# Kernel tuning notes

Hardware: AMD Instinct MI355X
Metric: run time of the kernel (lower is better)

Reference implementation:

```python
import jax, jax.numpy as jnp
import numpy as np

K = 20
EPS = 1e-5
NEG_SLOPE = 0.2


def _bn(x, gamma, beta, axes):
    # batch-norm in training mode (batch statistics), per-channel on last axis
    mean = jnp.mean(x, axis=axes, keepdims=True)
    var = jnp.var(x, axis=axes, keepdims=True)
    return gamma * (x - mean) * jax.lax.rsqrt(var + EPS) + beta


def _lrelu(x):
    return jnp.where(x >= 0, x, NEG_SLOPE * x)


def setup_inputs() -> dict:
    key = jax.random.key(0)
    ks = jax.random.split(key, 8)
    B, C, N = 8, 6, 4096

    def w(k_, shape):
        fan_in = shape[-1]
        return jax.random.normal(k_, shape, jnp.float32) / np.sqrt(fan_in)

    return {
        "x": jax.random.normal(ks[0], (B, C, N), jnp.float32),
        "conv1_w": w(ks[1], (64, 12)),
        "bn1_g": jnp.ones((64,), jnp.float32), "bn1_b": jnp.zeros((64,), jnp.float32),
        "conv2_w": w(ks[2], (128, 64)),
        "bn2_g": jnp.ones((128,), jnp.float32), "bn2_b": jnp.zeros((128,), jnp.float32),
        "conv3_w": w(ks[3], (1024, 128)),
        "bn3_g": jnp.ones((1024,), jnp.float32), "bn3_b": jnp.zeros((1024,), jnp.float32),
        "fc1_w": w(ks[4], (512, 1024)),
        "bn4_g": jnp.ones((512,), jnp.float32), "bn4_b": jnp.zeros((512,), jnp.float32),
        "fc2_w": w(ks[5], (256, 512)),
        "bn5_g": jnp.ones((256,), jnp.float32), "bn5_b": jnp.zeros((256,), jnp.float32),
        "fc3_w": w(ks[6], (9, 256)), "fc3_b": jnp.zeros((9,), jnp.float32),
        "fc4_w": w(ks[7], (3, 256)), "fc4_b": jnp.zeros((3,), jnp.float32),
    }


def _get_graph_feature(x, k):
    # x: [B, C, N] -> [B, N, k, 2C]
    B, C, N = x.shape
    xt = jnp.transpose(x, (0, 2, 1))                      # [B, N, C]
    xx = jnp.sum(xt * xt, axis=-1)                        # [B, N]
    inner = jnp.einsum('bnc,bmc->bnm', xt, xt)            # [B, N, N]
    pd = 2.0 * inner - xx[:, :, None] - xx[:, None, :]    # -||xi-xj||^2
    _, idx = jax.lax.top_k(pd, k)                         # [B, N, k]
    nbr = xt[jnp.arange(B)[:, None, None], idx]           # [B, N, k, C]
    center = jnp.broadcast_to(xt[:, :, None, :], nbr.shape)
    return jnp.concatenate([nbr - center, center], axis=-1)  # [B, N, k, 2C]


def reference(x, conv1_w, bn1_g, bn1_b, conv2_w, bn2_g, bn2_b,
              conv3_w, bn3_g, bn3_b, fc1_w, bn4_g, bn4_b,
              fc2_w, bn5_g, bn5_b, fc3_w, fc3_b, fc4_w, fc4_b):
    B = x.shape[0]
    feat = _get_graph_feature(x, K)                            # [B, N, k, 12]
    h = _lrelu(_bn(jnp.einsum('bnkc,oc->bnko', feat, conv1_w), bn1_g, bn1_b, (0, 1, 2)))
    h = _lrelu(_bn(jnp.einsum('bnkc,oc->bnko', h, conv2_w), bn2_g, bn2_b, (0, 1, 2)))
    h = jnp.max(h, axis=2)                                     # [B, N, 128] max over k
    h = _lrelu(_bn(jnp.einsum('bnc,oc->bno', h, conv3_w), bn3_g, bn3_b, (0, 1)))
    g = jnp.max(h, axis=1)                                     # [B, 1024] max over points
    g = _lrelu(_bn(g @ fc1_w.T, bn4_g, bn4_b, (0,)))           # [B, 512]
    g = _lrelu(_bn(g @ fc2_w.T, bn5_g, bn5_b, (0,)))           # [B, 256]
    bias = (g @ fc4_w.T + fc4_b)[:, None, :]                   # [B, 1, 3]
    matrix = jnp.eye(3, dtype=x.dtype) + (g @ fc3_w.T + fc3_b).reshape(B, 3, 3)
    xyz = jnp.transpose(x[:, :3, :], (0, 2, 1))                # [B, N, 3]
    out = jnp.einsum('bnc,bcd->bnd', xyz, matrix) + bias       # [B, N, 3]
    return jnp.transpose(out, (0, 2, 1))                       # [B, 3, N]
```

## Files before the change

kernel.cpp:

```cpp
#include <hip/hip_runtime.h>
#include <math.h>
#include <stddef.h>


static constexpr float EPS_ = 1e-5f;

__global__ __launch_bounds__(256) void k_prep(const float* __restrict__ x,
                                              float* __restrict__ xtp,
                                              const float* __restrict__ w2,
                                              float* __restrict__ w2t)
{
    int i = blockIdx.x*256 + threadIdx.x;
    int b = i >> 12, n = i & 4095;
    const float* xb = x + (size_t)b*6*4096 + n;
    float v0 = xb[0], v1 = xb[4096], v2 = xb[2*4096];
    float v3 = xb[3*4096], v4 = xb[4*4096], v5 = xb[5*4096];
    float xx = v0*v0 + v1*v1 + v2*v2 + v3*v3 + v4*v4 + v5*v5;
    float4* o = (float4*)(xtp + (size_t)i*8);
    o[0] = make_float4(v0, v1, v2, v3);
    o[1] = make_float4(v4, v5, xx, 0.f);
    if (blockIdx.x < 2){
        int e = blockIdx.x*256 + threadIdx.x;
        for (int q = e; q < 64*128; q += 512){
            int c = q >> 7, oo = q & 127;
            w2t[q] = w2[oo*64 + c];
        }
    }
}

__device__ __forceinline__ float pd_calc(const float4 a0, const float4 a1,
                                         const float4 q0, const float4 q1)
{
    float dot = a0.x*q0.x;
    dot = fmaf(a0.y, q0.y, dot);
    dot = fmaf(a0.z, q0.z, dot);
    dot = fmaf(a0.w, q0.w, dot);
    dot = fmaf(a1.x, q1.x, dot);
    dot = fmaf(a1.y, q1.y, dot);
    return fmaf(2.f, dot, -a1.z - q1.z);
}

__device__ __forceinline__ unsigned fkey_(float f){
    unsigned u = __float_as_uint(f);
    return (u & 0x80000000u) ? ~u : (u | 0x80000000u);
}
__device__ __forceinline__ float finv_(unsigned k){
    return (k & 0x80000000u) ? __uint_as_float(k & 0x7fffffffu)
                             : __uint_as_float(~k);
}

#define TK_CAP 384
__global__ __launch_bounds__(256) void k_topk(const float* __restrict__ xtp,
                                              int* __restrict__ idxout)
{
    __shared__ float maxs[4][256];
    __shared__ float candv[4][TK_CAP];
    __shared__ int   candi[4][TK_CAP];
    __shared__ float Ts[4];
    __shared__ unsigned ccnt[4], ocnt[4], nwork;
    __shared__ unsigned short work[1024];

    const int t = threadIdx.x;
    const int rowbase = blockIdx.x << 2;
    const int b = rowbase >> 12;
    const float* xb = xtp + ((size_t)b << 15);

    float4 c0[4], c1[4];
    #pragma unroll
    for (int c = 0; c < 4; c++){
        const float4* p = (const float4*)(xtp + (size_t)(rowbase + c)*8);
        c0[c] = p[0]; c1[c] = p[1];
    }
    if (t < 4){ ccnt[t] = 0u; ocnt[t] = 0u; }
    if (t == 0) nwork = 0u;

    float mx[4] = {-INFINITY, -INFINITY, -INFINITY, -INFINITY};
    {
        const float4* qp = (const float4*)(xb + (size_t)t*8);
        for (int i = 0; i < 16; i++){
            float4 q0 = qp[0], q1 = qp[1];
            #pragma unroll
            for (int c = 0; c < 4; c++)
                mx[c] = fmaxf(mx[c], pd_calc(c0[c], c1[c], q0, q1));
            qp += 512;
        }
    }
    #pragma unroll
    for (int c = 0; c < 4; c++) maxs[c][t] = mx[c];
    __syncthreads();

    const int w = t >> 6, lane = t & 63;
    {
        unsigned k0 = fkey_(maxs[w][lane]);
        unsigned k1 = fkey_(maxs[w][64  + lane]);
        unsigned k2 = fkey_(maxs[w][128 + lane]);
        unsigned k3 = fkey_(maxs[w][192 + lane]);
        unsigned lo = 0u;
        for (int bit = 31; bit >= 0; bit--){
            unsigned cand = lo | (1u << bit);
            int cnt = __popcll(__ballot(k0 >= cand))
                    + __popcll(__ballot(k1 >= cand))
                    + __popcll(__ballot(k2 >= cand))
                    + __popcll(__ballot(k3 >= cand));
            if (cnt >= 20) lo = cand;
        }
        if (lane == 0) Ts[w] = finv_(lo);
    }
    __syncthreads();

    #pragma unroll
    for (int c = 0; c < 4; c++){
        if (mx[c] >= Ts[c]){
            unsigned pos = atomicAdd(&nwork, 1u);
            work[pos] = (unsigned short)((c << 8) | t);
        }
    }
    __syncthreads();

    {
        int total = (int)nwork << 4;
        for (int e = t; e < total; e += 256){
            int ct = work[e >> 4];
            int c = ct >> 8, src = ct & 255;
            int m = ((e & 15) << 8) | src;
            const float4* p = (const float4*)(xb + (size_t)m*8);
            float4 q0 = p[0], q1 = p[1];
            float pd = pd_calc(c0[c], c1[c], q0, q1);
            if (pd >= Ts[c]){
                unsigned pos = atomicAdd(&ccnt[c], 1u);
                if (pos < TK_CAP){ candv[c][pos] = pd; candi[c][pos] = m; }
            }
        }
    }
    __syncthreads();

    {
        int n = (int)min(ccnt[w], (unsigned)TK_CAP);
        unsigned key[6]; int id[6];
        #pragma unroll
        for (int j = 0; j < 6; j++){
            int p = (j << 6) | lane;
            bool ok = p < n;
            key[j] = ok ? fkey_(candv[w][p]) : 0u;
            id[j]  = ok ? candi[w][p] : 0x7fffffff;
        }
        unsigned C = 0u;
        for (int bit = 31; bit >= 0; bit--){
            unsigned cand = C | (1u << bit);
            int cnt = 0;
            #pragma unroll
            for (int j = 0; j < 6; j++)
                cnt += __popcll(__ballot(key[j] >= cand));
            if (cnt >= 20) C = cand;
        }
        int m = 0, e = 0;
        #pragma unroll
        for (int j = 0; j < 6; j++){
            m += __popcll(__ballot(key[j] > C));
            e += __popcll(__ballot(key[j] == C));
        }
        int* outp = idxout + (size_t)(rowbase + w)*20;
        #pragma unroll
        for (int j = 0; j < 6; j++){
            if (key[j] > C){
                unsigned pos = atomicAdd(&ocnt[w], 1u);
                outp[pos] = id[j];
            }
        }
        int need = 20 - m;
        if (e <= need){
            #pragma unroll
            for (int j = 0; j < 6; j++){
                if (key[j] == C){
                    unsigned pos = atomicAdd(&ocnt[w], 1u);
                    outp[pos] = id[j];
                }
            }
        } else {
            for (int r = 0; r < need; r++){
                int loc = 0x7fffffff;
                #pragma unroll
                for (int j = 0; j < 6; j++)
                    if (key[j] == C && id[j] < loc) loc = id[j];
                int g = loc;
                #pragma unroll
                for (int s = 1; s < 64; s <<= 1) g = min(g, __shfl_xor(g, s));
                #pragma unroll
                for (int j = 0; j < 6; j++){
                    if (key[j] == C && id[j] == g){
                        key[j] = 0u;
                        unsigned pos = atomicAdd(&ocnt[w], 1u);
                        outp[pos] = g;
                    }
                }
            }
        }
    }
}

__global__ __launch_bounds__(256) void k_bn1stats(const float* __restrict__ xtp,
                                                  const int* __restrict__ idxb,
                                                  const float* __restrict__ w1,
                                                  float* __restrict__ bn1sum,
                                                  float* __restrict__ bn1sq)
{
    __shared__ float fT[320*12];
    __shared__ float red[2][4][64];
    const int t = threadIdx.x;
    const int rowbase = blockIdx.x << 4;
    const int b = rowbase >> 12;

    for (int s = t; s < 320; s += 256){
        int r = s / 20, k = s % 20;
        int grow = rowbase + r;
        int m = idxb[(size_t)grow*20 + k];
        const float4* pn = (const float4*)(xtp + (size_t)((b << 12) | m)*8);
        const float4* pc = (const float4*)(xtp + (size_t)grow*8);
        float4 n0 = pn[0], n1 = pn[1], c0 = pc[0], c1 = pc[1];
        float* f = fT + s*12;
        ((float4*)f)[0] = make_float4(n0.x-c0.x, n0.y-c0.y, n0.z-c0.z, n0.w-c0.w);
        ((float4*)f)[1] = make_float4(n1.x-c1.x, n1.y-c1.y, c0.x, c0.y);
        ((float4*)f)[2] = make_float4(c0.z, c0.w, c1.x, c1.y);
    }
    __syncthreads();
    const int o = t & 63, grp = t >> 6;
    float w[12];
    #pragma unroll
    for (int c = 0; c < 12; c++) w[c] = w1[o*12 + c];
    float sm = 0.f, sq = 0.f;
    for (int s = grp*80; s < grp*80 + 80; s++){
        const float* f = fT + s*12;
        float4 f0 = *(const float4*)(f);
        float4 fa = *(const float4*)(f + 4);
        float4 fb = *(const float4*)(f + 8);
        float h = w[0]*f0.x + w[1]*f0.y + w[2]*f0.z + w[3]*f0.w
                + w[4]*fa.x + w[5]*fa.y + w[6]*fa.z + w[7]*fa.w
                + w[8]*fb.x + w[9]*fb.y + w[10]*fb.z + w[11]*fb.w;
        sm += h; sq = fmaf(h, h, sq);
    }
    red[0][grp][o] = sm; red[1][grp][o] = sq;
    __syncthreads();
    if (t < 64){
        float a = red[0][0][t] + red[0][1][t] + red[0][2][t] + red[0][3][t];
        float c2 = red[1][0][t] + red[1][1][t] + red[1][2][t] + red[1][3][t];
        atomicAdd(bn1sum + t, a);
        atomicAdd(bn1sq + t, c2);
    }
}

__global__ void k_bnfin(const float* __restrict__ sum, const float* __restrict__ sq,
                        const float* __restrict__ gamma, const float* __restrict__ beta,
                        float* __restrict__ st, int C, float invN)
{
    int o = threadIdx.x;
    if (o < C){
        float mean = sum[o]*invN;
        float var  = sq[o]*invN - mean*mean;
        float s = gamma[o]/sqrtf(var + EPS_);
        st[o] = s;
        st[C + o] = beta[o] - mean*s;
    }
}

__global__ __launch_bounds__(256, 3) void k_conv12(
    const float* __restrict__ xtp, const int* __restrict__ idxb,
    const float* __restrict__ w1, const float* __restrict__ w2t,
    const float* __restrict__ bn1st,
    float* __restrict__ h2max, float* __restrict__ bn2sum, float* __restrict__ bn2sq)
{
    __shared__ float f1s[80*64];
    __shared__ float w2u[16*516];
    const int t = threadIdx.x;
    const int rowbase = blockIdx.x << 2;
    const int b = rowbase >> 12;

    const int jch = t & 63;
    float wr[12];
    #pragma unroll
    for (int c = 0; c < 12; c++) wr[c] = w1[jch*12 + c];

    float* fT = w2u;
    if (t < 80){
        int r = t / 20;
        int grow = rowbase + r;
        int m = idxb[(size_t)grow*20 + (t - r*20)];
        const float4* pn = (const float4*)(xtp + (size_t)((b << 12) | m)*8);
        const float4* pc = (const float4*)(xtp + (size_t)grow*8);
        float4 n0 = pn[0], n1 = pn[1], c0 = pc[0], c1 = pc[1];
        float* f = fT + t*12;
        ((float4*)f)[0] = make_float4(n0.x-c0.x, n0.y-c0.y, n0.z-c0.z, n0.w-c0.w);
        ((float4*)f)[1] = make_float4(n1.x-c1.x, n1.y-c1.y, c0.x, c0.y);
        ((float4*)f)[2] = make_float4(c0.z, c0.w, c1.x, c1.y);
    }
    __syncthreads();
    {
        const float s1 = bn1st[jch], t1 = bn1st[64 + jch];
        for (int vid = t; vid < 5120; vid += 256){
            int vec = vid >> 6;
            const float* f = fT + vec*12;
            float4 f0 = *(const float4*)(f);
            float4 fa = *(const float4*)(f + 4);
            float4 fb = *(const float4*)(f + 8);
            float acc = wr[0]*f0.x + wr[1]*f0.y + wr[2]*f0.z + wr[3]*f0.w
                      + wr[4]*fa.x + wr[5]*fa.y + wr[6]*fa.z + wr[7]*fa.w
                      + wr[8]*fb.x + wr[9]*fb.y + wr[10]*fb.z + wr[11]*fb.w;
            float v = fmaf(s1, acc, t1);
            f1s[(vec << 6) + (jch ^ ((vec & 7) << 2))] = fmaxf(v, 0.2f*v);
        }
    }
    __syncthreads();
    {
        float4 tmp[8];
        #pragma unroll
        for (int i = 0; i < 8; i++) tmp[i] = ((const float4*)w2t)[t + (i << 8)];
        #pragma unroll
        for (int i = 0; i < 8; i++){
            int q = t + (i << 8);
            int jr = q >> 5, o4 = q & 31;
            *(float4*)&w2u[(o4 >> 1)*516 + (jr << 3) + ((o4 & 1) << 2)] = tmp[i];
        }
    }
    __syncthreads();

    const int vg = t & 15, og = t >> 4;
    const float* fp = f1s + vg*5*64;
    const float* wp = w2u + og*516;
    int xw[5];
    #pragma unroll
    for (int i = 0; i < 5; i++) xw[i] = ((vg*5 + i) & 7) << 2;

    float h[5][8];
    #pragma unroll
    for (int i = 0; i < 5; i++)
        #pragma unroll
        for (int oi = 0; oi < 8; oi++) h[i][oi] = 0.f;

    #pragma unroll
    for (int jl = 0; jl < 64; jl += 4){
        float wv[4][8];
        #pragma unroll
        for (int jj = 0; jj < 4; jj++){
            *(float4*)&wv[jj][0] = *(const float4*)&wp[((jl + jj) << 3)];
            *(float4*)&wv[jj][4] = *(const float4*)&wp[((jl + jj) << 3) + 4];
        }
        #pragma unroll
        for (int i = 0; i < 5; i++){
            float fv[4];
            *(float4*)fv = *(const float4*)&fp[(i << 6) + (jl ^ xw[i])];
            #pragma unroll
            for (int jj = 0; jj < 4; jj++)
                #pragma unroll
                for (int oi = 0; oi < 8; oi++)
                    h[i][oi] = fmaf(fv[jj], wv[jj][oi], h[i][oi]);
        }
    }

    float mxl[8], sml[8], sql[8];
    #pragma unroll
    for (int oi = 0; oi < 8; oi++){
        float v = h[0][oi];
        mxl[oi] = v; sml[oi] = v; sql[oi] = v*v;
    }
    #pragma unroll
    for (int i = 1; i < 5; i++)
        #pragma unroll
        for (int oi = 0; oi < 8; oi++){
            float v = h[i][oi];
            mxl[oi] = fmaxf(mxl[oi], v);
            sml[oi] += v;
            sql[oi] = fmaf(v, v, sql[oi]);
        }
    __syncthreads();
    {
        const int r = vg >> 2, q = vg & 3;
        int base = (((q << 2) | r) << 7) + (og << 3);
        *(float4*)&w2u[base]        = *(float4*)&mxl[0];
        *(float4*)&w2u[base + 4]    = *(float4*)&mxl[4];
        *(float4*)&w2u[2048 + base]     = *(float4*)&sml[0];
        *(float4*)&w2u[2048 + base + 4] = *(float4*)&sml[4];
        *(float4*)&w2u[4096 + base]     = *(float4*)&sql[0];
        *(float4*)&w2u[4096 + base + 4] = *(float4*)&sql[4];
    }
    __syncthreads();
    for (int it = t; it < 512; it += 256){
        int r = it >> 7, o = it & 127;
        float m = w2u[(r << 7) + o];
        #pragma unroll
        for (int q = 1; q < 4; q++) m = fmaxf(m, w2u[(((q << 2) | r) << 7) + o]);
        h2max[(size_t)(rowbase + r)*128 + o] = m;
    }
    if (t < 128){
        float s = 0.f, qq = 0.f;
        #pragma unroll
        for (int u = 0; u < 16; u++){
            s  += w2u[2048 + (u << 7) + t];
            qq += w2u[4096 + (u << 7) + t];
        }
        atomicAdd(bn2sum + t, s);
        atomicAdd(bn2sq + t, qq);
    }
}

__global__ __launch_bounds__(256) void k_wt3(const float* __restrict__ w3,
                                             float* __restrict__ w3t)
{
    int i = blockIdx.x*256 + threadIdx.x;
    int j = i >> 10, o = i & 1023;
    w3t[i] = w3[(size_t)o*128 + j];
}

__global__ __launch_bounds__(256, 2) void k_conv3(const float* __restrict__ h2max,
    const float* __restrict__ bn2st, const float* __restrict__ w3t,
    float* __restrict__ bn3sum, float* __restrict__ bn3sq, unsigned int* __restrict__ gkey)
{
    __shared__ float f2[64*132];
    __shared__ float w3s[8192];
    const int t = threadIdx.x;
    const int bid = blockIdx.x;
    const int idx = bid >> 3;
    const int rt = (bid & 7)*64 + (idx >> 4);
    const int ot = idx & 15;
    const int rowbase = rt << 6;
    const int obase = ot << 6;
    const int b = rowbase >> 12;

    for (int e = t; e < 64*128; e += 256){
        int r = e >> 7, c = e & 127;
        float v = h2max[(size_t)(rowbase + r)*128 + c];
        float u = fmaf(bn2st[c], v, bn2st[128 + c]);
        f2[r*132 + c] = fmaxf(u, 0.2f*u);
    }
    {
        float4 tmp[8];
        #pragma unroll
        for (int i = 0; i < 8; i++){
            int q = t + (i << 8);
            tmp[i] = *(const float4*)&w3t[(size_t)(q >> 4)*1024 + obase + ((q & 15) << 2)];
        }
        #pragma unroll
        for (int i = 0; i < 8; i++) ((float4*)w3s)[t + (i << 8)] = tmp[i];
    }
    __syncthreads();

    const int oq = t & 15, rg = t >> 4;
    const int o0 = oq << 2, r0 = rg << 2;
    float h[4][4];
    #pragma unroll
    for (int rr = 0; rr < 4; rr++)
        #pragma unroll
        for (int oi = 0; oi < 4; oi++) h[rr][oi] = 0.f;

    for (int jl = 0; jl < 128; jl += 4){
        float wv[4][4];
        #pragma unroll
        for (int jj = 0; jj < 4; jj++)
            *(float4*)wv[jj] = *(const float4*)&w3s[(jl + jj)*64 + o0];
        float fr[4][4];
        #pragma unroll
        for (int rr = 0; rr < 4; rr++)
            *(float4*)fr[rr] = *(const float4*)&f2[(r0 + rr)*132 + jl];
        #pragma unroll
        for (int jj = 0; jj < 4; jj++)
            #pragma unroll
            for (int rr = 0; rr < 4; rr++)
                #pragma unroll
                for (int oi = 0; oi < 4; oi++)
                    h[rr][oi] = fmaf(fr[rr][jj], wv[jj][oi], h[rr][oi]);
    }

    float sml[4], sql[4], mxl[4];
    #pragma unroll
    for (int oi = 0; oi < 4; oi++){
        float v = h[0][oi];
        sml[oi] = v; sql[oi] = v*v; mxl[oi] = v;
    }
    #pragma unroll
    for (int rr = 1; rr < 4; rr++)
        #pragma unroll
        for (int oi = 0; oi < 4; oi++){
            float v = h[rr][oi];
            sml[oi] += v;
            sql[oi] = fmaf(v, v, sql[oi]);
            mxl[oi] = fmaxf(mxl[oi], v);
        }
    __syncthreads();
    float* scr = f2;
    *(float4*)&scr[(rg << 6) + o0]        = *(float4*)&sml[0];
    *(float4*)&scr[1024 + (rg << 6) + o0] = *(float4*)&sql[0];
    *(float4*)&scr[2048 + (rg << 6) + o0] = *(float4*)&mxl[0];
    __syncthreads();
    if (t < 192){
        int stat = t >> 6, o = t & 63;
        if (stat == 0){
            float s = 0.f;
            #pragma unroll
            for (int g2 = 0; g2 < 16; g2++) s += scr[(g2 << 6) + o];
            atomicAdd(bn3sum + obase + o, s);
        } else if (stat == 1){
            float s = 0.f;
            #pragma unroll
            for (int g2 = 0; g2 < 16; g2++) s += scr[1024 + (g2 << 6) + o];
            atomicAdd(bn3sq + obase + o, s);
        } else {
            float m = scr[2048 + o];
            #pragma unroll
            for (int g2 = 1; g2 < 16; g2++) m = fmaxf(m, scr[2048 + (g2 << 6) + o]);
            unsigned u = __float_as_uint(m);
            unsigned key = (u & 0x80000000u) ? ~u : (u | 0x80000000u);
            atomicMax(gkey + (b << 10) + obase + o, key);
        }
    }
}

__global__ void k_bn3g(const float* __restrict__ sum, const float* __restrict__ sq,
                       const unsigned int* __restrict__ gkey,
                       const float* __restrict__ gamma, const float* __restrict__ beta,
                       float* __restrict__ g)
{
    int o = blockIdx.x*256 + threadIdx.x;
    if (o < 1024){
        float mean = sum[o]*(1.f/32768.f);
        float var  = sq[o]*(1.f/32768.f) - mean*mean;
        float s = gamma[o]/sqrtf(var + EPS_);
        float tt = beta[o] - mean*s;
        for (int b = 0; b < 8; b++){
            unsigned k = gkey[(b << 10) + o];
            unsigned u = (k & 0x80000000u) ? (k & 0x7fffffffu) : ~k;
            float v = __uint_as_float(u);
            float xv = fmaf(s, v, tt);
            g[(b << 10) + o] = fmaxf(xv, 0.2f*xv);
        }
    }
}

__global__ __launch_bounds__(256) void k_fc(const float* __restrict__ in,
                                            const float* __restrict__ w,
                                            float* __restrict__ out, int Kdim, int Odim)
{
    int wid = (blockIdx.x*256 + threadIdx.x) >> 6;
    int lane = threadIdx.x & 63;
    int nout = 8*Odim;
    if (wid >= nout) return;
    int b = wid / Odim, o = wid - b*Odim;
    const float* gi = in + (size_t)b*Kdim;
    const float* wr = w + (size_t)o*Kdim;
    float acc = 0.f;
    for (int c = lane; c < Kdim; c += 64) acc = fmaf(gi[c], wr[c], acc);
    #pragma unroll
    for (int s = 32; s > 0; s >>= 1) acc += __shfl_xor(acc, s);
    if (lane == 0) out[(size_t)b*Odim + o] = acc;
}

__global__ void k_bnb(const float* __restrict__ h, const float* __restrict__ gamma,
                      const float* __restrict__ beta, float* __restrict__ g, int C)
{
    int o = blockIdx.x*256 + threadIdx.x;
    if (o < C){
        float s = 0.f, q = 0.f;
        for (int b = 0; b < 8; b++){ float v = h[(size_t)b*C + o]; s += v; q = fmaf(v, v, q); }
        float mean = s*0.125f;
        float var  = q*0.125f - mean*mean;
        float sc = gamma[o]/sqrtf(var + EPS_);
        float tt = beta[o] - mean*sc;
        for (int b = 0; b < 8; b++){
            float xv = fmaf(sc, h[(size_t)b*C + o], tt);
            g[(size_t)b*C + o] = fmaxf(xv, 0.2f*xv);
        }
    }
}

__global__ void k_head(const float* __restrict__ g5,
                       const float* __restrict__ fc3w, const float* __restrict__ fc3b,
                       const float* __restrict__ fc4w, const float* __restrict__ fc4b,
                       float* __restrict__ mat, float* __restrict__ bias3)
{
    int t = threadIdx.x;
    if (t < 96){
        int b = t / 12, j = t % 12;
        const float* gi = g5 + b*256;
        if (j < 9){
            const float* w = fc3w + j*256;
            float a = fc3b[j];
            for (int c = 0; c < 256; c++) a = fmaf(gi[c], w[c], a);
            if (j == 0 || j == 4 || j == 8) a += 1.f;
            mat[b*9 + j] = a;
        } else {
            int d = j - 9;
            const float* w = fc4w + d*256;
            float a = fc4b[d];
            for (int c = 0; c < 256; c++) a = fmaf(gi[c], w[c], a);
            bias3[b*3 + d] = a;
        }
    }
}

__global__ __launch_bounds__(256) void k_out(const float* __restrict__ x,
                                             const float* __restrict__ mat,
                                             const float* __restrict__ bias3,
                                             float* __restrict__ out)
{
    int i = blockIdx.x*256 + threadIdx.x;
    int n = i & 4095, bd = i >> 12;
    int b = bd / 3, d = bd - b*3;
    const float* xb = x + (size_t)b*6*4096 + n;
    const float* M = mat + b*9;
    out[i] = xb[0]*M[d] + xb[4096]*M[3 + d] + xb[2*4096]*M[6 + d] + bias3[b*3 + d];
}

extern "C" void kernel_launch(void* const* d_in, const int* in_sizes, int n_in,
                              void* d_out, int out_size, void* d_ws, size_t ws_size,
                              hipStream_t stream)
{
    const float* x     = (const float*)d_in[0];
    const float* w1    = (const float*)d_in[1];
    const float* bn1g  = (const float*)d_in[2];
    const float* bn1b  = (const float*)d_in[3];
    const float* w2    = (const float*)d_in[4];
    const float* bn2g  = (const float*)d_in[5];
    const float* bn2b  = (const float*)d_in[6];
    const float* w3    = (const float*)d_in[7];
    const float* bn3gm = (const float*)d_in[8];
    const float* bn3bt = (const float*)d_in[9];
    const float* fc1w  = (const float*)d_in[10];
    const float* bn4g  = (const float*)d_in[11];
    const float* bn4b  = (const float*)d_in[12];
    const float* fc2w  = (const float*)d_in[13];
    const float* bn5g  = (const float*)d_in[14];
    const float* bn5b  = (const float*)d_in[15];
    const float* fc3w  = (const float*)d_in[16];
    const float* fc3b  = (const float*)d_in[17];
    const float* fc4w  = (const float*)d_in[18];
    const float* fc4b  = (const float*)d_in[19];
    float* out = (float*)d_out;

    char* ws = (char*)d_ws;
    float* xtp   = (float*)(ws);
    float* w3t_g = (float*)(ws);
    int*   idxb  = (int*)  (ws + 1048576);
    float* h2max = (float*)(ws + 3670016);
    float* zs    = (float*)(ws + 20447232);
    float* bn1sum = zs;            float* bn1sq = zs + 64;
    float* bn2sum = zs + 128;      float* bn2sq = zs + 256;
    float* bn3sum = zs + 384;      float* bn3sq = zs + 1408;
    unsigned int* gkey = (unsigned int*)(zs + 2432);
    float* tail  = (float*)(ws + 20489728);
    float* bn1st = tail;
    float* bn2st = tail + 128;
    float* g     = tail + 384;
    float* h4    = tail + 8576;
    float* g4    = tail + 12672;
    float* h5    = tail + 16768;
    float* g5    = tail + 18816;
    float* mat   = tail + 20864;
    float* bias3 = tail + 20936;
    float* w2t_g = (float*)(ws + 20573568);

    hipMemsetAsync(zs, 0, 42496, stream);

    k_prep    <<<128,   256, 0, stream>>>(x, xtp, w2, w2t_g);
    k_topk    <<<8192,  256, 0, stream>>>(xtp, idxb);
    k_bn1stats<<<2048,  256, 0, stream>>>(xtp, idxb, w1, bn1sum, bn1sq);
    k_bnfin   <<<1,     128, 0, stream>>>(bn1sum, bn1sq, bn1g, bn1b, bn1st, 64, 1.f/655360.f);
    k_conv12  <<<8192,  256, 0, stream>>>(xtp, idxb, w1, w2t_g, bn1st, h2max, bn2sum, bn2sq);
    k_wt3     <<<512,   256, 0, stream>>>(w3, w3t_g);
    k_bnfin   <<<1,     128, 0, stream>>>(bn2sum, bn2sq, bn2g, bn2b, bn2st, 128, 1.f/655360.f);
    k_conv3   <<<8192,  256, 0, stream>>>(h2max, bn2st, w3t_g, bn3sum, bn3sq, gkey);
    k_bn3g    <<<4,     256, 0, stream>>>(bn3sum, bn3sq, gkey, bn3gm, bn3bt, g);
    k_fc      <<<1024,  256, 0, stream>>>(g, fc1w, h4, 1024, 512);
    k_bnb     <<<2,     256, 0, stream>>>(h4, bn4g, bn4b, g4, 512);
    k_fc      <<<512,   256, 0, stream>>>(g4, fc2w, h5, 512, 256);
    k_bnb     <<<1,     256, 0, stream>>>(h5, bn5g, bn5b, g5, 256);
    k_head    <<<1,     128, 0, stream>>>(g5, fc3w, fc3b, fc4w, fc4b, mat, bias3);
    k_out     <<<384,   256, 0, stream>>>(x, mat, bias3, out);
}
```

Before: 757.0 us.

## Process eight query rows per topk block and fold BN finalize into consumers

The top-k kernel now handles 8 rows per block instead of 4. Each thread computes max-pd for 8 rows from one pass of point loads, halving the candidate-point reads and the block count. Candidate collection and selection run in two passes of 4 rows so shared buffers stay the same size. Separately, the two single-block BN finalize kernels are removed and their per-channel scale/shift is recomputed inside conv12 and conv3, trading two launches for redundant per-block math and higher register pressure in topk.

```diff
diff --git a/kernel.cpp b/kernel.cpp
--- a/kernel.cpp
+++ b/kernel.cpp
@@ -53,48 +53,48 @@
 __global__ __launch_bounds__(256) void k_topk(const float* __restrict__ xtp,
                                               int* __restrict__ idxout)
 {
-    __shared__ float maxs[4][256];
+    __shared__ float maxs[8][256];
     __shared__ float candv[4][TK_CAP];
     __shared__ int   candi[4][TK_CAP];
-    __shared__ float Ts[4];
+    __shared__ float Ts[8];
     __shared__ unsigned ccnt[4], ocnt[4], nwork;
     __shared__ unsigned short work[1024];
 
     const int t = threadIdx.x;
-    const int rowbase = blockIdx.x << 2;
+    const int rowbase = blockIdx.x << 3;
     const int b = rowbase >> 12;
     const float* xb = xtp + ((size_t)b << 15);
 
-    float4 c0[4], c1[4];
-    #pragma unroll
-    for (int c = 0; c < 4; c++){
+    float4 c0[8], c1[8];
+    #pragma unroll
+    for (int c = 0; c < 8; c++){
         const float4* p = (const float4*)(xtp + (size_t)(rowbase + c)*8);
         c0[c] = p[0]; c1[c] = p[1];
     }
-    if (t < 4){ ccnt[t] = 0u; ocnt[t] = 0u; }
-    if (t == 0) nwork = 0u;
-
-    float mx[4] = {-INFINITY, -INFINITY, -INFINITY, -INFINITY};
+
+    float mx[8];
+    #pragma unroll
+    for (int c = 0; c < 8; c++) mx[c] = -INFINITY;
     {
         const float4* qp = (const float4*)(xb + (size_t)t*8);
         for (int i = 0; i < 16; i++){
             float4 q0 = qp[0], q1 = qp[1];
             #pragma unroll
-            for (int c = 0; c < 4; c++)
+            for (int c = 0; c < 8; c++)
                 mx[c] = fmaxf(mx[c], pd_calc(c0[c], c1[c], q0, q1));
             qp += 512;
         }
     }
     #pragma unroll
-    for (int c = 0; c < 4; c++) maxs[c][t] = mx[c];
+    for (int c = 0; c < 8; c++) maxs[c][t] = mx[c];
     __syncthreads();
 
     const int w = t >> 6, lane = t & 63;
-    {
-        unsigned k0 = fkey_(maxs[w][lane]);
-        unsigned k1 = fkey_(maxs[w][64  + lane]);
-        unsigned k2 = fkey_(maxs[w][128 + lane]);
-        unsigned k3 = fkey_(maxs[w][192 + lane]);
+    for (int cc = w; cc < 8; cc += 4){
+        unsigned k0 = fkey_(maxs[cc][lane]);
+        unsigned k1 = fkey_(maxs[cc][64  + lane]);
+        unsigned k2 = fkey_(maxs[cc][128 + lane]);
+        unsigned k3 = fkey_(maxs[cc][192 + lane]);
         unsigned lo = 0u;
         for (int bit = 31; bit >= 0; bit--){
             unsigned cand = lo | (1u << bit);
@@ -104,97 +104,105 @@
                     + __popcll(__ballot(k3 >= cand));
             if (cnt >= 20) lo = cand;
         }
-        if (lane == 0) Ts[w] = finv_(lo);
-    }
-    __syncthreads();
-
-    #pragma unroll
-    for (int c = 0; c < 4; c++){
-        if (mx[c] >= Ts[c]){
-            unsigned pos = atomicAdd(&nwork, 1u);
-            work[pos] = (unsigned short)((c << 8) | t);
-        }
-    }
-    __syncthreads();
-
-    {
-        int total = (int)nwork << 4;
-        for (int e = t; e < total; e += 256){
-            int ct = work[e >> 4];
-            int c = ct >> 8, src = ct & 255;
-            int m = ((e & 15) << 8) | src;
-            const float4* p = (const float4*)(xb + (size_t)m*8);
-            float4 q0 = p[0], q1 = p[1];
-            float pd = pd_calc(c0[c], c1[c], q0, q1);
-            if (pd >= Ts[c]){
-                unsigned pos = atomicAdd(&ccnt[c], 1u);
-                if (pos < TK_CAP){ candv[c][pos] = pd; candi[c][pos] = m; }
+        if (lane == 0) Ts[cc] = finv_(lo);
+    }
+    __syncthreads();
+
+    for (int p = 0; p < 2; p++){
+        const int cb = p << 2;
+        if (t < 4){ ccnt[t] = 0u; ocnt[t] = 0u; }
+        if (t == 0) nwork = 0u;
+        __syncthreads();
+
+        #pragma unroll
+        for (int c = 0; c < 4; c++){
+            if (mx[cb + c] >= Ts[cb + c]){
+                unsigned pos = atomicAdd(&nwork, 1u);
+                work[pos] = (unsigned short)((c << 8) | t);
             }
         }
-    }
-    __syncthreads();
-
-    {
-        int n = (int)min(ccnt[w], (unsigned)TK_CAP);
-        unsigned key[6]; int id[6];
-        #pragma unroll
-        for (int j = 0; j < 6; j++){
-            int p = (j << 6) | lane;
-            bool ok = p < n;
-            key[j] = ok ? fkey_(candv[w][p]) : 0u;
-            id[j]  = ok ? candi[w][p] : 0x7fffffff;
-        }
-        unsigned C = 0u;
-        for (int bit = 31; bit >= 0; bit--){
-            unsigned cand = C | (1u << bit);
-            int cnt = 0;
-            #pragma unroll
-            for (int j = 0; j < 6; j++)
-                cnt += __popcll(__ballot(key[j] >= cand));
-            if (cnt >= 20) C = cand;
-        }
-        int m = 0, e = 0;
-        #pragma unroll
-        for (int j = 0; j < 6; j++){
-            m += __popcll(__ballot(key[j] > C));
-            e += __popcll(__ballot(key[j] == C));
-        }
-        int* outp = idxout + (size_t)(rowbase + w)*20;
-        #pragma unroll
-        for (int j = 0; j < 6; j++){
-            if (key[j] > C){
-                unsigned pos = atomicAdd(&ocnt[w], 1u);
-                outp[pos] = id[j];
+        __syncthreads();
+
+        {
+            int total = (int)nwork << 4;
+            for (int e = t; e < total; e += 256){
+                int ct = work[e >> 4];
+                int c = ct >> 8, src = ct & 255;
+                int m = ((e & 15) << 8) | src;
+                const float4* pp = (const float4*)(xb + (size_t)m*8);
+                float4 q0 = pp[0], q1 = pp[1];
+                float pd = pd_calc(c0[cb + c], c1[cb + c], q0, q1);
+                if (pd >= Ts[cb + c]){
+                    unsigned pos = atomicAdd(&ccnt[c], 1u);
+                    if (pos < TK_CAP){ candv[c][pos] = pd; candi[c][pos] = m; }
+                }
             }
         }
-        int need = 20 - m;
-        if (e <= need){
+        __syncthreads();
+
+        {
+            int n = (int)min(ccnt[w], (unsigned)TK_CAP);
+            unsigned key[6]; int id[6];
             #pragma unroll
             for (int j = 0; j < 6; j++){
-                if (key[j] == C){
+                int pz = (j << 6) | lane;
+                bool ok = pz < n;
+                key[j] = ok ? fkey_(candv[w][pz]) : 0u;
+                id[j]  = ok ? candi[w][pz] : 0x7fffffff;
+            }
+            unsigned C = 0u;
+            for (int bit = 31; bit >= 0; bit--){
+                unsigned cand = C | (1u << bit);
+                int cnt = 0;
+                #pragma unroll
+                for (int j = 0; j < 6; j++)
+                    cnt += __popcll(__ballot(key[j] >= cand));
+                if (cnt >= 20) C = cand;
+            }
+            int m = 0, e = 0;
+            #pragma unroll
+            for (int j = 0; j < 6; j++){
+                m += __popcll(__ballot(key[j] > C));
+                e += __popcll(__ballot(key[j] == C));
+            }
+            int* outp = idxout + (size_t)(rowbase + cb + w)*20;
+            #pragma unroll
+            for (int j = 0; j < 6; j++){
+                if (key[j] > C){
                     unsigned pos = atomicAdd(&ocnt[w], 1u);
                     outp[pos] = id[j];
                 }
             }
-        } else {
-            for (int r = 0; r < need; r++){
-                int loc = 0x7fffffff;
-                #pragma unroll
-                for (int j = 0; j < 6; j++)
-                    if (key[j] == C && id[j] < loc) loc = id[j];
-                int g = loc;
-                #pragma unroll
-                for (int s = 1; s < 64; s <<= 1) g = min(g, __shfl_xor(g, s));
+            int need = 20 - m;
+            if (e <= need){
                 #pragma unroll
                 for (int j = 0; j < 6; j++){
-                    if (key[j] == C && id[j] == g){
-                        key[j] = 0u;
+                    if (key[j] == C){
                         unsigned pos = atomicAdd(&ocnt[w], 1u);
-                        outp[pos] = g;
+                        outp[pos] = id[j];
+                    }
+                }
+            } else {
+                for (int r = 0; r < need; r++){
+                    int loc = 0x7fffffff;
+                    #pragma unroll
+                    for (int j = 0; j < 6; j++)
+                        if (key[j] == C && id[j] < loc) loc = id[j];
+                    int g = loc;
+                    #pragma unroll
+                    for (int s = 1; s < 64; s <<= 1) g = min(g, __shfl_xor(g, s));
+                    #pragma unroll
+                    for (int j = 0; j < 6; j++){
+                        if (key[j] == C && id[j] == g){
+                            key[j] = 0u;
+                            unsigned pos = atomicAdd(&ocnt[w], 1u);
+                            outp[pos] = g;
+                        }
                     }
                 }
             }
         }
+        __syncthreads();
     }
 }
 
@@ -248,24 +256,11 @@
     }
 }
 
-__global__ void k_bnfin(const float* __restrict__ sum, const float* __restrict__ sq,
-                        const float* __restrict__ gamma, const float* __restrict__ beta,
-                        float* __restrict__ st, int C, float invN)
-{
-    int o = threadIdx.x;
-    if (o < C){
-        float mean = sum[o]*invN;
-        float var  = sq[o]*invN - mean*mean;
-        float s = gamma[o]/sqrtf(var + EPS_);
-        st[o] = s;
-        st[C + o] = beta[o] - mean*s;
-    }
-}
-
 __global__ __launch_bounds__(256, 3) void k_conv12(
     const float* __restrict__ xtp, const int* __restrict__ idxb,
     const float* __restrict__ w1, const float* __restrict__ w2t,
-    const float* __restrict__ bn1st,
+    const float* __restrict__ bn1sum, const float* __restrict__ bn1sq,
+    const float* __restrict__ bn1g, const float* __restrict__ bn1b,
     float* __restrict__ h2max, float* __restrict__ bn2sum, float* __restrict__ bn2sq)
 {
     __shared__ float f1s[80*64];
@@ -278,6 +273,13 @@
     float wr[12];
     #pragma unroll
     for (int c = 0; c < 12; c++) wr[c] = w1[jch*12 + c];
+    float s1, t1;
+    {
+        float mean = bn1sum[jch]*(1.f/655360.f);
+        float var  = bn1sq[jch]*(1.f/655360.f) - mean*mean;
+        s1 = bn1g[jch]/sqrtf(var + EPS_);
+        t1 = bn1b[jch] - mean*s1;
+    }
 
     float* fT = w2u;
     if (t < 80){
@@ -294,7 +296,6 @@
     }
     __syncthreads();
     {
-        const float s1 = bn1st[jch], t1 = bn1st[64 + jch];
         for (int vid = t; vid < 5120; vid += 256){
             int vec = vid >> 6;
             const float* f = fT + vec*12;
@@ -410,11 +411,14 @@
 }
 
 __global__ __launch_bounds__(256, 2) void k_conv3(const float* __restrict__ h2max,
-    const float* __restrict__ bn2st, const float* __restrict__ w3t,
+    const float* __restrict__ bn2sum, const float* __restrict__ bn2sq,
+    const float* __restrict__ bn2g, const float* __restrict__ bn2b,
+    const float* __restrict__ w3t,
     float* __restrict__ bn3sum, float* __restrict__ bn3sq, unsigned int* __restrict__ gkey)
 {
     __shared__ float f2[64*132];
     __shared__ float w3s[8192];
+    __shared__ float bn2stL[256];
     const int t = threadIdx.x;
     const int bid = blockIdx.x;
     const int idx = bid >> 3;
@@ -424,10 +428,19 @@
     const int obase = ot << 6;
     const int b = rowbase >> 12;
 
+    if (t < 128){
+        float mean = bn2sum[t]*(1.f/655360.f);
+        float var  = bn2sq[t]*(1.f/655360.f) - mean*mean;
+        float s = bn2g[t]/sqrtf(var + EPS_);
+        bn2stL[t] = s;
+        bn2stL[128 + t] = bn2b[t] - mean*s;
+    }
+    __syncthreads();
+
     for (int e = t; e < 64*128; e += 256){
         int r = e >> 7, c = e & 127;
         float v = h2max[(size_t)(rowbase + r)*128 + c];
-        float u = fmaf(bn2st[c], v, bn2st[128 + c]);
+        float u = fmaf(bn2stL[c], v, bn2stL[128 + c]);
         f2[r*132 + c] = fmaxf(u, 0.2f*u);
     }
     {
@@ -644,27 +657,26 @@
     float* bn3sum = zs + 384;      float* bn3sq = zs + 1408;
     unsigned int* gkey = (unsigned int*)(zs + 2432);
     float* tail  = (float*)(ws + 20489728);
-    float* bn1st = tail;
-    float* bn2st = tail + 128;
-    float* g     = tail + 384;
-    float* h4    = tail + 8576;
-    float* g4    = tail + 12672;
-    float* h5    = tail + 16768;
-    float* g5    = tail + 18816;
-    float* mat   = tail + 20864;
-    float* bias3 = tail + 20936;
+    float* g     = tail;
+    float* h4    = tail + 8192;
+    float* g4    = tail + 12288;
+    float* h5    = tail + 16384;
+    float* g5    = tail + 18432;
+    float* mat   = tail + 20480;
+    float* bias3 = tail + 20552;
     float* w2t_g = (float*)(ws + 20573568);
 
     hipMemsetAsync(zs, 0, 42496, stream);
 
     k_prep    <<<128,   256, 0, stream>>>(x, xtp, w2, w2t_g);
-    k_topk    <<<8192,  256, 0, stream>>>(xtp, idxb);
+    k_topk    <<<4096,  256, 0, stream>>>(xtp, idxb);
     k_bn1stats<<<2048,  256, 0, stream>>>(xtp, idxb, w1, bn1sum, bn1sq);
-    k_bnfin   <<<1,     128, 0, stream>>>(bn1sum, bn1sq, bn1g, bn1b, bn1st, 64, 1.f/655360.f);
-    k_conv12  <<<8192,  256, 0, stream>>>(xtp, idxb, w1, w2t_g, bn1st, h2max, bn2sum, bn2sq);
+    k_conv12  <<<8192,  256, 0, stream>>>(xtp, idxb, w1, w2t_g,
+                                          bn1sum, bn1sq, bn1g, bn1b,
+                                          h2max, bn2sum, bn2sq);
     k_wt3     <<<512,   256, 0, stream>>>(w3, w3t_g);
-    k_bnfin   <<<1,     128, 0, stream>>>(bn2sum, bn2sq, bn2g, bn2b, bn2st, 128, 1.f/655360.f);
-    k_conv3   <<<8192,  256, 0, stream>>>(h2max, bn2st, w3t_g, bn3sum, bn3sq, gkey);
+    k_conv3   <<<8192,  256, 0, stream>>>(h2max, bn2sum, bn2sq, bn2g, bn2b,
+                                          w3t_g, bn3sum, bn3sq, gkey);
     k_bn3g    <<<4,     256, 0, stream>>>(bn3sum, bn3sq, gkey, bn3gm, bn3bt, g);
     k_fc      <<<1024,  256, 0, stream>>>(g, fc1w, h4, 1024, 512);
     k_bnb     <<<2,     256, 0, stream>>>(h4, bn4g, bn4b, g4, 512);
```

Result: faster. 725.1 us (-4.2%).
